# Kernel tuning notes

Measured on AMD Instinct MI355X. Metric: run time of the kernel, lower is better.

The kernel has to match this reference:

```python
import jax, jax.numpy as jnp
import numpy as np

RBF_SIGMA = 0.5
K_CTRL = 128
BN_EPS = 1e-5


def farthest_point_sampling(points, K):
    """points: (B,N,3) -> indices (B,K) int32. Sequential FPS via lax.scan."""
    B, N, _ = points.shape
    d0 = jnp.full((B, N), jnp.inf, dtype=points.dtype)
    far0 = jnp.zeros((B,), dtype=jnp.int32)

    def step(carry, _):
        dmin, far = carry
        centroid = jnp.take_along_axis(points, far[:, None, None], axis=1)  # (B,1,3)
        d = jnp.sum((points - centroid) ** 2, axis=-1)                      # (B,N)
        dmin = jnp.minimum(dmin, d)
        far = jnp.argmax(dmin, axis=-1).astype(jnp.int32)
        return (dmin, far), far

    _, rest = jax.lax.scan(step, (d0, far0), None, length=K - 1)  # rest: (K-1,B)
    return jnp.concatenate([far0[:, None], rest.T], axis=1)       # (B,K)


def _bn_relu(h, g, b):
    # BatchNorm1d in training mode: biased batch stats over rows.
    mu = h.mean(axis=0)
    var = h.var(axis=0)
    return jax.nn.relu(g * (h - mu) * jax.lax.rsqrt(var + BN_EPS) + b)


def setup_inputs() -> dict:
    key = jax.random.key(0)
    ks = jax.random.split(key, 12)
    B, N, M, F, H = 8, 16384, 16384, 1024, 512
    inp = {
        "source_rigid_2": jax.random.normal(ks[0], (B, N, 3), jnp.float32),
        "per_point_feats": jax.random.normal(ks[1], (B, N, F), jnp.float32),
        "tgt_points": jax.random.normal(ks[2], (B, M, 3), jnp.float32),
        "tgt_point_feats": jax.random.normal(ks[3], (B, M, F), jnp.float32),
        "W1": jax.random.normal(ks[4], (2 * F, H), jnp.float32) * (1.0 / np.sqrt(2 * F)),
        "b1": jnp.zeros((H,), jnp.float32),
        "g1": jnp.ones((H,), jnp.float32),
        "beta1": jnp.zeros((H,), jnp.float32),
        "W2": jax.random.normal(ks[5], (H, H), jnp.float32) * (1.0 / np.sqrt(H)),
        "b2": jnp.zeros((H,), jnp.float32),
        "g2": jnp.ones((H,), jnp.float32),
        "beta2": jnp.zeros((H,), jnp.float32),
        "W3": jnp.zeros((H, 3), jnp.float32),   # zero-init last layer (as in torch)
        "b3": jnp.zeros((3,), jnp.float32),
    }
    return inp


def reference(source_rigid_2, per_point_feats, tgt_points, tgt_point_feats,
              W1, b1, g1, beta1, W2, b2, g2, beta2, W3, b3):
    B, N, _ = source_rigid_2.shape
    K = min(K_CTRL, N)

    # 1. FPS control point selection
    cp_idx = farthest_point_sampling(source_rigid_2, K)                     # (B,K)
    control_points = jnp.take_along_axis(source_rigid_2, cp_idx[..., None], axis=1)  # (B,K,3)
    control_feats = jnp.take_along_axis(per_point_feats, cp_idx[..., None], axis=1)  # (B,K,F)

    # 2. nearest target point per control point (squared dists; argmin == cdist argmin)
    cp2 = jnp.sum(control_points ** 2, axis=-1, keepdims=True)              # (B,K,1)
    tg2 = jnp.sum(tgt_points ** 2, axis=-1)[:, None, :]                     # (B,1,M)
    cross = jnp.einsum('bkd,bmd->bkm', control_points, tgt_points)
    nn_idx = jnp.argmin(cp2 + tg2 - 2.0 * cross, axis=-1)                   # (B,K)
    tgt_local_feats = jnp.take_along_axis(tgt_point_feats, nn_idx[..., None], axis=1)  # (B,K,F)

    # 3. displacement MLP on (B*K, 2F)
    mlp_in = jnp.concatenate([control_feats, tgt_local_feats], axis=-1).reshape(B * K, -1)
    h = _bn_relu(mlp_in @ W1 + b1, g1, beta1)
    h = _bn_relu(h @ W2 + b2, g2, beta2)
    w = (h @ W3 + b3).reshape(B, K, 3)                                      # control displacements

    # 4. RBF-softmax interpolation to all N points
    diff = source_rigid_2[:, :, None, :] - control_points[:, None, :, :]    # (B,N,K,3)
    sq_dists = jnp.sum(diff ** 2, axis=-1)                                  # (B,N,K)
    weights = jax.nn.softmax(-sq_dists / (2.0 * RBF_SIGMA ** 2), axis=-1)
    delta = jnp.einsum('bnk,bkd->bnd', weights, w)
    output = source_rigid_2 + delta
    return output, delta, control_points, w
```

## Files before the change

### kernel.cpp

```cpp
#include <hip/hip_runtime.h>
#include <hip/hip_bf16.h>

#define FPS_THREADS 1024
#define FPS_PAIRS 8
#define CONV_BLOCKS 120

typedef __attribute__((ext_vector_type(8))) short bf16x8;
typedef __attribute__((ext_vector_type(4))) float f32x4;
typedef __attribute__((ext_vector_type(2))) float f32x2;

__device__ inline unsigned long long shfl_down_u64(unsigned long long x, int off) {
    unsigned int lo = (unsigned int)(x & 0xFFFFFFFFull);
    unsigned int hi = (unsigned int)(x >> 32);
    lo = __shfl_down(lo, off, 64);
    hi = __shfl_down(hi, off, 64);
    return (((unsigned long long)hi) << 32) | lo;
}

__device__ inline unsigned short f2bf(float x) {
    union { float f; unsigned int u; } v; v.f = x;
    unsigned int r = v.u + 0x7FFFu + ((v.u >> 16) & 1u);
    return (unsigned short)(r >> 16);
}

__device__ inline float wave_max_dpp(float v) {
    int w = __float_as_int(v);
#define DPP_MAX_STEP(ctrl, rmask)                                             \
    {                                                                         \
        int _t = __builtin_amdgcn_update_dpp(w, w, ctrl, rmask, 0xf, false);  \
        w = __float_as_int(fmaxf(__int_as_float(w), __int_as_float(_t)));     \
    }
    DPP_MAX_STEP(0x111, 0xf)
    DPP_MAX_STEP(0x112, 0xf)
    DPP_MAX_STEP(0x114, 0xf)
    DPP_MAX_STEP(0x118, 0xf)
    DPP_MAX_STEP(0x142, 0xa)
    DPP_MAX_STEP(0x143, 0xc)
#undef DPP_MAX_STEP
    return __int_as_float(__builtin_amdgcn_readlane(w, 63));
}

__global__ __launch_bounds__(FPS_THREADS) void fps_conv_kernel(
        const float* __restrict__ src, int* __restrict__ cp_idx,
        float* __restrict__ out_cp,
        const float* __restrict__ W1, const float* __restrict__ W2,
        unsigned short* __restrict__ W1t, unsigned short* __restrict__ W2t,
        float* __restrict__ stats, int N, int K) {
    const int t = threadIdx.x;
    if (blockIdx.x >= 8) {
        const int cb = blockIdx.x - 8;
        if (cb == 0) { stats[t] = 0.f; stats[t + 1024] = 0.f; }
        for (size_t idx = (size_t)cb * 1024 + t; idx < (size_t)2048 * 512;
             idx += (size_t)CONV_BLOCKS * 1024) {
            int k = (int)(idx >> 9), n = (int)(idx & 511);
            W1t[(size_t)n * 2048 + k] = f2bf(W1[idx]);
        }
        for (size_t idx = (size_t)cb * 1024 + t; idx < (size_t)512 * 512;
             idx += (size_t)CONV_BLOCKS * 1024) {
            int k = (int)(idx >> 9), n = (int)(idx & 511);
            W2t[(size_t)n * 512 + k] = f2bf(W2[idx]);
        }
        return;
    }

    const int b = blockIdx.x;
    const float* p = src + (size_t)b * N * 3;

    f32x2 px2[FPS_PAIRS], py2[FPS_PAIRS], pz2[FPS_PAIRS], dm2[FPS_PAIRS];
#pragma unroll
    for (int a = 0; a < FPS_PAIRS; ++a) {
        int j0 = (2 * a) * FPS_THREADS + t;
        int j1 = (2 * a + 1) * FPS_THREADS + t;
        px2[a] = (f32x2){p[j0 * 3 + 0], p[j1 * 3 + 0]};
        py2[a] = (f32x2){p[j0 * 3 + 1], p[j1 * 3 + 1]};
        pz2[a] = (f32x2){p[j0 * 3 + 2], p[j1 * 3 + 2]};
        dm2[a] = (f32x2){__builtin_huge_valf(), __builtin_huge_valf()};
    }

    __shared__ unsigned long long slot[3];
    if (t == 0) { slot[0] = 0ull; slot[1] = 0ull; slot[2] = 0ull; }
    __syncthreads();

    int far = 0;
    int cur = 0;
    for (int k = 0;; ++k) {
        const float cx = p[far * 3 + 0];
        const float cy = p[far * 3 + 1];
        const float cz = p[far * 3 + 2];
        if (t == 0) {
            cp_idx[b * K + k] = far;
            out_cp[(b * K + k) * 3 + 0] = cx;
            out_cp[(b * K + k) * 3 + 1] = cy;
            out_cp[(b * K + k) * 3 + 2] = cz;
        }
        if (k == K - 1) break;

        const f32x2 vcx = (f32x2){cx, cx};
        const f32x2 vcy = (f32x2){cy, cy};
        const f32x2 vcz = (f32x2){cz, cz};

#pragma unroll
        for (int a = 0; a < FPS_PAIRS; ++a) {
            f32x2 dx = px2[a] - vcx;
            f32x2 dy = py2[a] - vcy;
            f32x2 dz = pz2[a] - vcz;
            f32x2 d = dx * dx;
            d += dy * dy;
            d += dz * dz;
            f32x2 dm = dm2[a];
            dm.x = fminf(dm.x, d.x);
            dm.y = fminf(dm.y, d.y);
            dm2[a] = dm;
        }
        float tmax = -1.0f;
        int jbest = 0;
#pragma unroll
        for (int a = 0; a < FPS_PAIRS; ++a) {
            f32x2 dm = dm2[a];
            bool c0 = dm.x > tmax;
            tmax = c0 ? dm.x : tmax;
            jbest = c0 ? ((2 * a) * FPS_THREADS + t) : jbest;
            bool c1 = dm.y > tmax;
            tmax = c1 ? dm.y : tmax;
            jbest = c1 ? ((2 * a + 1) * FPS_THREADS + t) : jbest;
        }

        const float wmax = wave_max_dpp(tmax);
        if (tmax == wmax) {
            unsigned long long pk =
                (((unsigned long long)__float_as_uint(wmax)) << 32) |
                (unsigned long long)(0xFFFFFFFFu - (unsigned int)jbest);
            atomicMax(&slot[cur], pk);
        }
        const int nxt = (cur == 2) ? 0 : cur + 1;
        if (t == 0) slot[nxt] = 0ull;
        __syncthreads();
        unsigned long long bb = slot[cur];
        far = (int)(0xFFFFFFFFu - (unsigned int)(bb & 0xFFFFFFFFull));
        cur = nxt;
    }
}

__global__ __launch_bounds__(256) void nn_gather(
        const float* __restrict__ tgt, const float* __restrict__ cp,
        const int* __restrict__ cp_idx,
        const float* __restrict__ src_feats, const float* __restrict__ tgt_feats,
        unsigned short* __restrict__ mlp_b, int N, int M, int F) {
    const int bk = blockIdx.x;
    const int b = bk >> 7;
    const int t = threadIdx.x;
    const float* tp = tgt + (size_t)b * M * 3;

    const float cx = cp[bk * 3 + 0], cy = cp[bk * 3 + 1], cz = cp[bk * 3 + 2];
    const float cp2 = cx * cx + cy * cy + cz * cz;

    unsigned long long best = ~0ull;
#pragma unroll 4
    for (int m = t; m < M; m += 256) {
        float tx = tp[m * 3 + 0], ty = tp[m * 3 + 1], tz = tp[m * 3 + 2];
        float tg2 = tx * tx + ty * ty + tz * tz;
        float cross = cx * tx + cy * ty + cz * tz;
        float v = (cp2 + tg2) - 2.0f * cross;
        unsigned int fb = __float_as_uint(v);
        fb = (fb & 0x80000000u) ? ~fb : (fb | 0x80000000u);
        unsigned long long pk = (((unsigned long long)fb) << 32) | (unsigned int)m;
        best = (pk < best) ? pk : best;
    }
#pragma unroll
    for (int off = 32; off >= 1; off >>= 1) {
        unsigned long long o = shfl_down_u64(best, off);
        best = (o < best) ? o : best;
    }
    __shared__ unsigned long long red[4];
    __shared__ int snn;
    if ((t & 63) == 0) red[t >> 6] = best;
    __syncthreads();
    if (t == 0) {
        unsigned long long bb = red[0];
        for (int wv = 1; wv < 4; ++wv) bb = (red[wv] < bb) ? red[wv] : bb;
        snn = (int)(bb & 0xFFFFFFFFull);
    }
    __syncthreads();
    const int nn = snn;

    const float4* a = reinterpret_cast<const float4*>(
        src_feats + ((size_t)b * N + cp_idx[bk]) * F);
    const float4* c = reinterpret_cast<const float4*>(
        tgt_feats + ((size_t)b * M + nn) * F);
    unsigned short* o = mlp_b + (size_t)bk * 2 * F;
    float4 av = a[t];
    float4 cv = c[t];
    ushort4 a4, c4;
    a4.x = f2bf(av.x); a4.y = f2bf(av.y); a4.z = f2bf(av.z); a4.w = f2bf(av.w);
    c4.x = f2bf(cv.x); c4.y = f2bf(cv.y); c4.z = f2bf(cv.z); c4.w = f2bf(cv.w);
    *reinterpret_cast<ushort4*>(&o[t * 4]) = a4;
    *reinterpret_cast<ushort4*>(&o[F + t * 4]) = c4;
}

__global__ __launch_bounds__(256) void gemm_mfma_stats(
        const unsigned short* __restrict__ A, const unsigned short* __restrict__ Bt,
        const float* __restrict__ bias, float* __restrict__ C,
        float* __restrict__ psum, float* __restrict__ psumsq,
        int M, int N, int K) {
    __shared__ __align__(16) unsigned short As[64][72];
    __shared__ __align__(16) unsigned short Bs[64][72];
    __shared__ float sS[64], sSS[64];
    const int tid = threadIdx.x;
    const int w = tid >> 6, l = tid & 63;
    const int m0 = blockIdx.y * 64, n0 = blockIdx.x * 64;

    f32x4 acc[4];
#pragma unroll
    for (int nt = 0; nt < 4; ++nt) acc[nt] = (f32x4){0.f, 0.f, 0.f, 0.f};

    const int lr = l & 15;
    const int lg = l >> 4;

    for (int kt = 0; kt < K; kt += 64) {
        __syncthreads();
#pragma unroll
        for (int s = 0; s < 2; ++s) {
            int u = tid + s * 256;
            int row = u >> 3, kc = (u & 7) * 8;
            *reinterpret_cast<uint4*>(&As[row][kc]) =
                *reinterpret_cast<const uint4*>(&A[(size_t)(m0 + row) * K + kt + kc]);
            *reinterpret_cast<uint4*>(&Bs[row][kc]) =
                *reinterpret_cast<const uint4*>(&Bt[(size_t)(n0 + row) * K + kt + kc]);
        }
        __syncthreads();
#pragma unroll
        for (int kf = 0; kf < 2; ++kf) {
            bf16x8 af = *reinterpret_cast<const bf16x8*>(&As[w * 16 + lr][kf * 32 + lg * 8]);
#pragma unroll
            for (int nt = 0; nt < 4; ++nt) {
                bf16x8 bfr = *reinterpret_cast<const bf16x8*>(&Bs[nt * 16 + lr][kf * 32 + lg * 8]);
                acc[nt] = __builtin_amdgcn_mfma_f32_16x16x32_bf16(af, bfr, acc[nt], 0, 0, 0);
            }
        }
    }

    if (tid < 64) { sS[tid] = 0.f; sSS[tid] = 0.f; }
    __syncthreads();
#pragma unroll
    for (int nt = 0; nt < 4; ++nt) {
        const int col = n0 + nt * 16 + lr;
        const float bv = bias[col];
        float s = 0.f, ss = 0.f;
#pragma unroll
        for (int r = 0; r < 4; ++r) {
            const int row = m0 + w * 16 + lg * 4 + r;
            float v = acc[nt][r] + bv;
            C[(size_t)row * N + col] = v;
            s += v; ss += v * v;
        }
        s += __shfl_xor(s, 16, 64); ss += __shfl_xor(ss, 16, 64);
        s += __shfl_xor(s, 32, 64); ss += __shfl_xor(ss, 32, 64);
        if (lg == 0) {
            atomicAdd(&sS[nt * 16 + lr], s);
            atomicAdd(&sSS[nt * 16 + lr], ss);
        }
    }
    __syncthreads();
    if (tid < 64) {
        atomicAdd(&psum[n0 + tid], sS[tid]);
        atomicAdd(&psumsq[n0 + tid], sSS[tid]);
    }
}

__global__ __launch_bounds__(256) void bn_apply_bf16(
        const float* __restrict__ Hm, const float* __restrict__ psum,
        const float* __restrict__ psumsq, const float* __restrict__ g,
        const float* __restrict__ beta, unsigned short* __restrict__ out,
        float invM) {
    const int i = (blockIdx.x * 256 + threadIdx.x) * 4;
    float4 x = *reinterpret_cast<const float4*>(&Hm[i]);
    const int c = i & 511;
    ushort4 o4;
    float xv[4] = {x.x, x.y, x.z, x.w};
    unsigned short ov[4];
#pragma unroll
    for (int j = 0; j < 4; ++j) {
        const int col = c + j;
        const float m = psum[col] * invM;
        const float var = fmaxf(psumsq[col] * invM - m * m, 0.f);
        const float rs = rsqrtf(var + 1e-5f);
        float h = fmaxf(g[col] * (xv[j] - m) * rs + beta[col], 0.f);
        ov[j] = f2bf(h);
    }
    o4.x = ov[0]; o4.y = ov[1]; o4.z = ov[2]; o4.w = ov[3];
    *reinterpret_cast<ushort4*>(&out[i]) = o4;
}

__global__ __launch_bounds__(256) void bn_head(
        const float* __restrict__ H2, const float* __restrict__ psum,
        const float* __restrict__ psumsq, const float* __restrict__ g,
        const float* __restrict__ beta, const float* __restrict__ W3,
        const float* __restrict__ b3, float* __restrict__ w_out,
        int Ncols, float invM) {
    const int r = blockIdx.x;
    const int t = threadIdx.x;
    float a0 = 0.f, a1 = 0.f, a2 = 0.f;
    for (int c = t; c < Ncols; c += 256) {
        const float m = psum[c] * invM;
        const float var = fmaxf(psumsq[c] * invM - m * m, 0.f);
        const float rs = rsqrtf(var + 1e-5f);
        float x = H2[(size_t)r * Ncols + c];
        float h = fmaxf(g[c] * (x - m) * rs + beta[c], 0.f);
        a0 += h * W3[c * 3 + 0];
        a1 += h * W3[c * 3 + 1];
        a2 += h * W3[c * 3 + 2];
    }
#pragma unroll
    for (int off = 32; off >= 1; off >>= 1) {
        a0 += __shfl_down(a0, off, 64);
        a1 += __shfl_down(a1, off, 64);
        a2 += __shfl_down(a2, off, 64);
    }
    __shared__ float red[4][3];
    if ((t & 63) == 0) {
        red[t >> 6][0] = a0; red[t >> 6][1] = a1; red[t >> 6][2] = a2;
    }
    __syncthreads();
    if (t == 0) {
        float s0 = red[0][0] + red[1][0] + red[2][0] + red[3][0];
        float s1 = red[0][1] + red[1][1] + red[2][1] + red[3][1];
        float s2 = red[0][2] + red[1][2] + red[2][2] + red[3][2];
        w_out[r * 3 + 0] = s0 + b3[0];
        w_out[r * 3 + 1] = s1 + b3[1];
        w_out[r * 3 + 2] = s2 + b3[2];
    }
}

__global__ __launch_bounds__(256) void rbf_kernel(
        const float* __restrict__ src, const float* __restrict__ cp,
        const float* __restrict__ w, float* __restrict__ outp,
        float* __restrict__ delta, int N, int K) {
    __shared__ float scx[128], scy[128], scz[128];
    __shared__ float swx[128], swy[128], swz[128];
    const int b = blockIdx.x >> 6;
    const int chunk = blockIdx.x & 63;
    const int t = threadIdx.x;
    if (t < K) {
        const int base = (b * K + t) * 3;
        scx[t] = cp[base + 0]; scy[t] = cp[base + 1]; scz[t] = cp[base + 2];
        swx[t] = w[base + 0];  swy[t] = w[base + 1];  swz[t] = w[base + 2];
    }
    __syncthreads();

    const int n = chunk * 256 + t;
    const size_t pbase = ((size_t)b * N + n) * 3;
    const float x = src[pbase + 0], y = src[pbase + 1], z = src[pbase + 2];

    float mind = __builtin_huge_valf();
    for (int k = 0; k < K; ++k) {
        float dx = x - scx[k], dy = y - scy[k], dz = z - scz[k];
        float d2 = dx * dx + dy * dy + dz * dz;
        mind = fminf(mind, d2);
    }
    float sum = 0.f, ax = 0.f, ay = 0.f, az = 0.f;
    for (int k = 0; k < K; ++k) {
        float dx = x - scx[k], dy = y - scy[k], dz = z - scz[k];
        float d2 = dx * dx + dy * dy + dz * dz;
        float e = __expf(2.0f * (mind - d2));
        sum += e;
        ax += e * swx[k]; ay += e * swy[k]; az += e * swz[k];
    }
    const float inv = 1.0f / sum;
    ax *= inv; ay *= inv; az *= inv;
    delta[pbase + 0] = ax; delta[pbase + 1] = ay; delta[pbase + 2] = az;
    outp[pbase + 0] = x + ax; outp[pbase + 1] = y + ay; outp[pbase + 2] = z + az;
}

extern "C" void kernel_launch(void* const* d_in, const int* in_sizes, int n_in,
                              void* d_out, int out_size, void* d_ws, size_t ws_size,
                              hipStream_t stream) {
    const int B = 8, N = 16384, M = 16384, F = 1024, H = 512, K = 128;
    const int BK = B * K;

    const float* src       = (const float*)d_in[0];
    const float* ppf       = (const float*)d_in[1];
    const float* tgt       = (const float*)d_in[2];
    const float* tpf       = (const float*)d_in[3];
    const float* W1        = (const float*)d_in[4];
    const float* b1        = (const float*)d_in[5];
    const float* g1        = (const float*)d_in[6];
    const float* beta1     = (const float*)d_in[7];
    const float* W2        = (const float*)d_in[8];
    const float* b2        = (const float*)d_in[9];
    const float* g2        = (const float*)d_in[10];
    const float* beta2     = (const float*)d_in[11];
    const float* W3        = (const float*)d_in[12];
    const float* b3        = (const float*)d_in[13];

    float* out_output = (float*)d_out;
    float* out_delta  = out_output + (size_t)B * N * 3;
    float* out_cp     = out_delta + (size_t)B * N * 3;
    float* out_w      = out_cp + (size_t)B * K * 3;

    char* ws = (char*)d_ws;
    int*            cp_idx = (int*)(ws + 0);
    float*          stats  = (float*)(ws + 4096);
    float* psum1   = stats;
    float* psumsq1 = stats + 512;
    float* psum2   = stats + 1024;
    float* psumsq2 = stats + 1536;
    unsigned short* mlp_b  = (unsigned short*)(ws + 16384);
    unsigned short* W1t    = (unsigned short*)(ws + 4210688);
    unsigned short* W2t    = (unsigned short*)(ws + 6307840);
    float*          h1     = (float*)(ws + 6832128);
    unsigned short* h1b    = (unsigned short*)(ws + 8929280);
    float*          h2     = (float*)(ws + 9977856);

    fps_conv_kernel<<<8 + CONV_BLOCKS, FPS_THREADS, 0, stream>>>(
        src, cp_idx, out_cp, W1, W2, W1t, W2t, stats, N, K);
    nn_gather<<<BK, 256, 0, stream>>>(tgt, out_cp, cp_idx, ppf, tpf, mlp_b, N, M, F);
    gemm_mfma_stats<<<dim3(H / 64, BK / 64), 256, 0, stream>>>(
        mlp_b, W1t, b1, h1, psum1, psumsq1, BK, H, 2 * F);
    bn_apply_bf16<<<(BK * H / 4) / 256, 256, 0, stream>>>(
        h1, psum1, psumsq1, g1, beta1, h1b, 1.0f / BK);
    gemm_mfma_stats<<<dim3(H / 64, BK / 64), 256, 0, stream>>>(
        h1b, W2t, b2, h2, psum2, psumsq2, BK, H, H);
    bn_head<<<BK, 256, 0, stream>>>(
        h2, psum2, psumsq2, g2, beta2, W3, b3, out_w, H, 1.0f / BK);
    rbf_kernel<<<B * (N / 256), 256, 0, stream>>>(src, out_cp, out_w, out_output, out_delta, N, K);
}
```

Baseline: 316.3 us.

## Fuse BN1 apply into GEMM2 and fold BN2+head into RBF kernel

Folds the first BatchNorm+ReLU+bf16 conversion into the A-tile load of the second GEMM, and moves BN2 plus the W3 head into the RBF interpolation kernel. This removes two kernel launches and the h1b intermediate round trip. In exchange, each of the 512 RBF blocks recomputes the full 128x512 head for its batch, re-reading h2 (256KB per block) redundantly.

Measured after the change: 341.2 us. 7.9% more time.

```diff
diff --git a/kernel.cpp b/kernel.cpp
--- a/kernel.cpp
+++ b/kernel.cpp
@@ -267,103 +267,199 @@
     }
 }
 
-__global__ __launch_bounds__(256) void bn_apply_bf16(
-        const float* __restrict__ Hm, const float* __restrict__ psum,
-        const float* __restrict__ psumsq, const float* __restrict__ g,
-        const float* __restrict__ beta, unsigned short* __restrict__ out,
-        float invM) {
-    const int i = (blockIdx.x * 256 + threadIdx.x) * 4;
-    float4 x = *reinterpret_cast<const float4*>(&Hm[i]);
-    const int c = i & 511;
-    ushort4 o4;
-    float xv[4] = {x.x, x.y, x.z, x.w};
-    unsigned short ov[4];
-#pragma unroll
-    for (int j = 0; j < 4; ++j) {
-        const int col = c + j;
-        const float m = psum[col] * invM;
-        const float var = fmaxf(psumsq[col] * invM - m * m, 0.f);
-        const float rs = rsqrtf(var + 1e-5f);
-        float h = fmaxf(g[col] * (xv[j] - m) * rs + beta[col], 0.f);
-        ov[j] = f2bf(h);
-    }
-    o4.x = ov[0]; o4.y = ov[1]; o4.z = ov[2]; o4.w = ov[3];
-    *reinterpret_cast<ushort4*>(&out[i]) = o4;
-}
-
-__global__ __launch_bounds__(256) void bn_head(
-        const float* __restrict__ H2, const float* __restrict__ psum,
-        const float* __restrict__ psumsq, const float* __restrict__ g,
-        const float* __restrict__ beta, const float* __restrict__ W3,
-        const float* __restrict__ b3, float* __restrict__ w_out,
-        int Ncols, float invM) {
-    const int r = blockIdx.x;
-    const int t = threadIdx.x;
-    float a0 = 0.f, a1 = 0.f, a2 = 0.f;
-    for (int c = t; c < Ncols; c += 256) {
-        const float m = psum[c] * invM;
-        const float var = fmaxf(psumsq[c] * invM - m * m, 0.f);
-        const float rs = rsqrtf(var + 1e-5f);
-        float x = H2[(size_t)r * Ncols + c];
-        float h = fmaxf(g[c] * (x - m) * rs + beta[c], 0.f);
-        a0 += h * W3[c * 3 + 0];
-        a1 += h * W3[c * 3 + 1];
-        a2 += h * W3[c * 3 + 2];
-    }
-#pragma unroll
-    for (int off = 32; off >= 1; off >>= 1) {
-        a0 += __shfl_down(a0, off, 64);
-        a1 += __shfl_down(a1, off, 64);
-        a2 += __shfl_down(a2, off, 64);
-    }
-    __shared__ float red[4][3];
-    if ((t & 63) == 0) {
-        red[t >> 6][0] = a0; red[t >> 6][1] = a1; red[t >> 6][2] = a2;
-    }
-    __syncthreads();
-    if (t == 0) {
-        float s0 = red[0][0] + red[1][0] + red[2][0] + red[3][0];
-        float s1 = red[0][1] + red[1][1] + red[2][1] + red[3][1];
-        float s2 = red[0][2] + red[1][2] + red[2][2] + red[3][2];
-        w_out[r * 3 + 0] = s0 + b3[0];
-        w_out[r * 3 + 1] = s1 + b3[1];
-        w_out[r * 3 + 2] = s2 + b3[2];
-    }
-}
-
-__global__ __launch_bounds__(256) void rbf_kernel(
+__global__ __launch_bounds__(256) void gemm2_fused(
+        const float* __restrict__ h1, const unsigned short* __restrict__ Bt,
+        const float* __restrict__ bias, float* __restrict__ C,
+        const float* __restrict__ psum1, const float* __restrict__ psumsq1,
+        const float* __restrict__ g1, const float* __restrict__ beta1,
+        float* __restrict__ psum2, float* __restrict__ psumsq2,
+        int M, int N, int K) {
+    __shared__ __align__(16) unsigned short As[64][72];
+    __shared__ __align__(16) unsigned short Bs[64][72];
+    __shared__ float sS[64], sSS[64];
+    __shared__ float sc1[512], sh1[512];
+    const int tid = threadIdx.x;
+    const int w = tid >> 6, l = tid & 63;
+    const int m0 = blockIdx.y * 64, n0 = blockIdx.x * 64;
+    const float invM = 1.0f / 1024.0f;
+
+    for (int c = tid; c < 512; c += 256) {
+        float m = psum1[c] * invM;
+        float var = fmaxf(psumsq1[c] * invM - m * m, 0.f);
+        float rs = rsqrtf(var + 1e-5f);
+        float sc = g1[c] * rs;
+        sc1[c] = sc;
+        sh1[c] = beta1[c] - m * sc;
+    }
+
+    f32x4 acc[4];
+#pragma unroll
+    for (int nt = 0; nt < 4; ++nt) acc[nt] = (f32x4){0.f, 0.f, 0.f, 0.f};
+
+    const int lr = l & 15;
+    const int lg = l >> 4;
+
+    for (int kt = 0; kt < K; kt += 64) {
+        __syncthreads();
+#pragma unroll
+        for (int s = 0; s < 4; ++s) {
+            int u = tid + s * 256;
+            int row = u >> 4, cg = (u & 15) * 4;
+            float4 x = *reinterpret_cast<const float4*>(
+                &h1[(size_t)(m0 + row) * K + kt + cg]);
+            float xv[4] = {x.x, x.y, x.z, x.w};
+            ushort4 o;
+            unsigned short ov[4];
+#pragma unroll
+            for (int j = 0; j < 4; ++j) {
+                int col = kt + cg + j;
+                float v = fmaxf(fmaf(sc1[col], xv[j], sh1[col]), 0.f);
+                ov[j] = f2bf(v);
+            }
+            o.x = ov[0]; o.y = ov[1]; o.z = ov[2]; o.w = ov[3];
+            *reinterpret_cast<ushort4*>(&As[row][cg]) = o;
+        }
+#pragma unroll
+        for (int s = 0; s < 2; ++s) {
+            int u = tid + s * 256;
+            int row = u >> 3, kc = (u & 7) * 8;
+            *reinterpret_cast<uint4*>(&Bs[row][kc]) =
+                *reinterpret_cast<const uint4*>(&Bt[(size_t)(n0 + row) * K + kt + kc]);
+        }
+        __syncthreads();
+#pragma unroll
+        for (int kf = 0; kf < 2; ++kf) {
+            bf16x8 af = *reinterpret_cast<const bf16x8*>(&As[w * 16 + lr][kf * 32 + lg * 8]);
+#pragma unroll
+            for (int nt = 0; nt < 4; ++nt) {
+                bf16x8 bfr = *reinterpret_cast<const bf16x8*>(&Bs[nt * 16 + lr][kf * 32 + lg * 8]);
+                acc[nt] = __builtin_amdgcn_mfma_f32_16x16x32_bf16(af, bfr, acc[nt], 0, 0, 0);
+            }
+        }
+    }
+
+    if (tid < 64) { sS[tid] = 0.f; sSS[tid] = 0.f; }
+    __syncthreads();
+#pragma unroll
+    for (int nt = 0; nt < 4; ++nt) {
+        const int col = n0 + nt * 16 + lr;
+        const float bv = bias[col];
+        float s = 0.f, ss = 0.f;
+#pragma unroll
+        for (int r = 0; r < 4; ++r) {
+            const int row = m0 + w * 16 + lg * 4 + r;
+            float v = acc[nt][r] + bv;
+            C[(size_t)row * N + col] = v;
+            s += v; ss += v * v;
+        }
+        s += __shfl_xor(s, 16, 64); ss += __shfl_xor(ss, 16, 64);
+        s += __shfl_xor(s, 32, 64); ss += __shfl_xor(ss, 32, 64);
+        if (lg == 0) {
+            atomicAdd(&sS[nt * 16 + lr], s);
+            atomicAdd(&sSS[nt * 16 + lr], ss);
+        }
+    }
+    __syncthreads();
+    if (tid < 64) {
+        atomicAdd(&psum2[n0 + tid], sS[tid]);
+        atomicAdd(&psumsq2[n0 + tid], sSS[tid]);
+    }
+}
+
+__global__ __launch_bounds__(256) void rbf_w_kernel(
         const float* __restrict__ src, const float* __restrict__ cp,
-        const float* __restrict__ w, float* __restrict__ outp,
+        const float* __restrict__ h2,
+        const float* __restrict__ psum2, const float* __restrict__ psumsq2,
+        const float* __restrict__ g2, const float* __restrict__ beta2,
+        const float* __restrict__ W3, const float* __restrict__ b3,
+        float* __restrict__ out_w, float* __restrict__ outp,
         float* __restrict__ delta, int N, int K) {
-    __shared__ float scx[128], scy[128], scz[128];
-    __shared__ float swx[128], swy[128], swz[128];
+    __shared__ float tile[16][520];
+    __shared__ float sc2[512], sh2[512];
+    __shared__ float sW3[512][3];
+    __shared__ float sw[128][3];
+    __shared__ float spt[128][3];
+
     const int b = blockIdx.x >> 6;
     const int chunk = blockIdx.x & 63;
     const int t = threadIdx.x;
-    if (t < K) {
-        const int base = (b * K + t) * 3;
-        scx[t] = cp[base + 0]; scy[t] = cp[base + 1]; scz[t] = cp[base + 2];
-        swx[t] = w[base + 0];  swy[t] = w[base + 1];  swz[t] = w[base + 2];
-    }
-    __syncthreads();
+    const float invM = 1.0f / 1024.0f;
+
+    for (int c = t; c < 512; c += 256) {
+        float m = psum2[c] * invM;
+        float var = fmaxf(psumsq2[c] * invM - m * m, 0.f);
+        float rs = rsqrtf(var + 1e-5f);
+        float sc = g2[c] * rs;
+        sc2[c] = sc;
+        sh2[c] = beta2[c] - m * sc;
+    }
+    for (int i = t; i < 512 * 3; i += 256) sW3[i / 3][i % 3] = W3[i];
+    if (t < 128) {
+        const int base = (b * 128 + t) * 3;
+        spt[t][0] = cp[base + 0]; spt[t][1] = cp[base + 1]; spt[t][2] = cp[base + 2];
+    }
+    __syncthreads();
+
+    const int row16 = t >> 4;
+    const int g = t & 15;
+    const float b30 = b3[0], b31 = b3[1], b32 = b3[2];
+    for (int tb = 0; tb < 8; ++tb) {
+        const int r0 = tb * 16;
+#pragma unroll
+        for (int s = 0; s < 8; ++s) {
+            int lin = s * 1024 + t * 4;
+            int row = lin >> 9, col = lin & 511;
+            *reinterpret_cast<float4*>(&tile[row][col]) =
+                *reinterpret_cast<const float4*>(
+                    &h2[((size_t)(b * 128 + r0 + row)) * 512 + col]);
+        }
+        __syncthreads();
+        float a0 = 0.f, a1 = 0.f, a2 = 0.f;
+#pragma unroll 8
+        for (int i = 0; i < 32; ++i) {
+            int c = g + i * 16;
+            float h = fmaxf(fmaf(sc2[c], tile[row16][c], sh2[c]), 0.f);
+            a0 += h * sW3[c][0];
+            a1 += h * sW3[c][1];
+            a2 += h * sW3[c][2];
+        }
+#pragma unroll
+        for (int off = 8; off >= 1; off >>= 1) {
+            a0 += __shfl_down(a0, off, 64);
+            a1 += __shfl_down(a1, off, 64);
+            a2 += __shfl_down(a2, off, 64);
+        }
+        if (g == 0) {
+            sw[r0 + row16][0] = a0 + b30;
+            sw[r0 + row16][1] = a1 + b31;
+            sw[r0 + row16][2] = a2 + b32;
+        }
+        __syncthreads();
+    }
+    if (chunk == 0 && t < 128) {
+        const int base = (b * 128 + t) * 3;
+        out_w[base + 0] = sw[t][0];
+        out_w[base + 1] = sw[t][1];
+        out_w[base + 2] = sw[t][2];
+    }
 
     const int n = chunk * 256 + t;
     const size_t pbase = ((size_t)b * N + n) * 3;
     const float x = src[pbase + 0], y = src[pbase + 1], z = src[pbase + 2];
 
     float mind = __builtin_huge_valf();
-    for (int k = 0; k < K; ++k) {
-        float dx = x - scx[k], dy = y - scy[k], dz = z - scz[k];
+    for (int k = 0; k < 128; ++k) {
+        float dx = x - spt[k][0], dy = y - spt[k][1], dz = z - spt[k][2];
         float d2 = dx * dx + dy * dy + dz * dz;
         mind = fminf(mind, d2);
     }
     float sum = 0.f, ax = 0.f, ay = 0.f, az = 0.f;
-    for (int k = 0; k < K; ++k) {
-        float dx = x - scx[k], dy = y - scy[k], dz = z - scz[k];
+    for (int k = 0; k < 128; ++k) {
+        float dx = x - spt[k][0], dy = y - spt[k][1], dz = z - spt[k][2];
         float d2 = dx * dx + dy * dy + dz * dz;
         float e = __expf(2.0f * (mind - d2));
         sum += e;
-        ax += e * swx[k]; ay += e * swy[k]; az += e * swz[k];
+        ax += e * sw[k][0]; ay += e * sw[k][1]; az += e * sw[k][2];
     }
     const float inv = 1.0f / sum;
     ax *= inv; ay *= inv; az *= inv;
@@ -408,7 +504,6 @@
     unsigned short* W1t    = (unsigned short*)(ws + 4210688);
     unsigned short* W2t    = (unsigned short*)(ws + 6307840);
     float*          h1     = (float*)(ws + 6832128);
-    unsigned short* h1b    = (unsigned short*)(ws + 8929280);
     float*          h2     = (float*)(ws + 9977856);
 
     fps_conv_kernel<<<8 + CONV_BLOCKS, FPS_THREADS, 0, stream>>>(
@@ -416,11 +511,9 @@
     nn_gather<<<BK, 256, 0, stream>>>(tgt, out_cp, cp_idx, ppf, tpf, mlp_b, N, M, F);
     gemm_mfma_stats<<<dim3(H / 64, BK / 64), 256, 0, stream>>>(
         mlp_b, W1t, b1, h1, psum1, psumsq1, BK, H, 2 * F);
-    bn_apply_bf16<<<(BK * H / 4) / 256, 256, 0, stream>>>(
-        h1, psum1, psumsq1, g1, beta1, h1b, 1.0f / BK);
-    gemm_mfma_stats<<<dim3(H / 64, BK / 64), 256, 0, stream>>>(
-        h1b, W2t, b2, h2, psum2, psumsq2, BK, H, H);
-    bn_head<<<BK, 256, 0, stream>>>(
-        h2, psum2, psumsq2, g2, beta2, W3, b3, out_w, H, 1.0f / BK);
-    rbf_kernel<<<B * (N / 256), 256, 0, stream>>>(src, out_cp, out_w, out_output, out_delta, N, K);
-}
+    gemm2_fused<<<dim3(H / 64, BK / 64), 256, 0, stream>>>(
+        h1, W2t, b2, h2, psum1, psumsq1, g1, beta1, psum2, psumsq2, BK, H, H);
+    rbf_w_kernel<<<B * (N / 256), 256, 0, stream>>>(
+        src, out_cp, h2, psum2, psumsq2, g2, beta2, W3, b3,
+        out_w, out_output, out_delta, N, K);
+}
```
